# Optimization experiments

Hardware: AMD Instinct MI355X
Metric: run time of the kernel (lower is better)

## Reference

```python
import jax, jax.numpy as jnp
import numpy as np

N, E, IN, H, C, EDIM, G, NC = 20000, 200000, 512, 4, 64, 384, 64, 751
NEG_GATV2 = 0.2   # leaky_relu slope inside GATv2 attention
NEG_ACT = 0.01    # F.leaky_relu default between layers


def _w(key, shape):
    return jax.random.normal(key, shape, dtype=jnp.float32) * 0.05


def setup_inputs() -> dict:
    key = jax.random.key(0)
    ks = jax.random.split(key, 24)
    x = jax.random.normal(ks[0], (N, IN), dtype=jnp.float32)
    edge_index = jax.random.randint(ks[1], (2, E), 0, N, dtype=jnp.int32)
    edge_attr = jax.random.normal(ks[2], (E, EDIM), dtype=jnp.float32)
    batch = (jnp.arange(N, dtype=jnp.int32) * G) // N  # sorted, covers all G graphs
    return {
        "x": x, "edge_index": edge_index, "edge_attr": edge_attr, "batch": batch,
        # GATv2 layer 1 (512 -> 4 heads x 64, concat)
        "W1l": _w(ks[3], (IN, H * C)), "b1l": jnp.zeros((H * C,), jnp.float32),
        "W1r": _w(ks[4], (IN, H * C)), "b1r": jnp.zeros((H * C,), jnp.float32),
        "W1e": _w(ks[5], (EDIM, H * C)),
        "att1": _w(ks[6], (H, C)), "bias1": jnp.zeros((H * C,), jnp.float32),
        # GATv2 layer 2 (256 -> 1 head x 64)
        "W2l": _w(ks[7], (H * C, C)), "b2l": jnp.zeros((C,), jnp.float32),
        "W2r": _w(ks[8], (H * C, C)), "b2r": jnp.zeros((C,), jnp.float32),
        "W2e": _w(ks[9], (EDIM, C)),
        "att2": _w(ks[10], (1, C)), "bias2": jnp.zeros((C,), jnp.float32),
        # LayerNorm + classifier
        "ln_g": jnp.ones((C,), jnp.float32), "ln_b": jnp.zeros((C,), jnp.float32),
        "clf_W": _w(ks[11], (C, NC)), "clf_b": jnp.zeros((NC,), jnp.float32),
    }


def gatv2_layer(x, ei_i, ei_j, ea, Wl, bl, Wr, br, We, att, bias, heads, outc):
    n = x.shape[0]
    xl = (x @ Wl + bl).reshape(n, heads, outc)  # source-side transform (x_j)
    xr = (x @ Wr + br).reshape(n, heads, outc)  # target-side transform (x_i)
    ep = (ea @ We).reshape(-1, heads, outc)     # lin_edge has no bias in PyG
    m = jax.nn.leaky_relu(xl[ei_j] + xr[ei_i] + ep, NEG_GATV2)  # [E',H,C]
    logit = jnp.einsum('ehc,hc->eh', m, att)
    lmax = jax.ops.segment_max(logit, ei_i, num_segments=n)
    ex = jnp.exp(logit - lmax[ei_i])
    den = jax.ops.segment_sum(ex, ei_i, num_segments=n)
    alpha = ex / den[ei_i]                                       # segment softmax
    out = jax.ops.segment_sum(xl[ei_j] * alpha[:, :, None], ei_i, num_segments=n)
    return out.reshape(n, heads * outc) + bias, alpha


def reference(x, edge_index, edge_attr, batch, W1l, b1l, W1r, b1r, W1e, att1, bias1,
              W2l, b2l, W2r, b2r, W2e, att2, bias2, ln_g, ln_b, clf_W, clf_b):
    n = x.shape[0]
    row, col = edge_index[0], edge_index[1]
    # add_self_loops with fill_value='mean': loop attr = scatter-mean over edge_index[1]
    cnt = jax.ops.segment_sum(jnp.ones_like(edge_attr[:, 0]), col, num_segments=n)
    loop_attr = jax.ops.segment_sum(edge_attr, col, num_segments=n) / jnp.maximum(cnt, 1.0)[:, None]
    loops = jnp.arange(n, dtype=row.dtype)
    # flow='target_to_source': aggregate at i=edge_index[0], messages from j=edge_index[1]
    ei_i = jnp.concatenate([row, loops])
    ei_j = jnp.concatenate([col, loops])
    ea = jnp.concatenate([edge_attr, loop_attr], axis=0)

    h1, _ = gatv2_layer(x, ei_i, ei_j, ea, W1l, b1l, W1r, b1r, W1e, att1, bias1, H, C)
    h1 = jax.nn.leaky_relu(h1, NEG_ACT)
    h2, _ = gatv2_layer(h1, ei_i, ei_j, ea, W2l, b2l, W2r, b2r, W2e, att2, bias2, 1, C)
    h2 = jax.nn.leaky_relu(h2, NEG_ACT)

    g = jax.ops.segment_max(h2, batch, num_segments=G)  # global_max_pool -> [G, C]
    mu = g.mean(axis=-1, keepdims=True)
    var = g.var(axis=-1, keepdims=True)
    gn = (g - mu) / jnp.sqrt(var + 1e-5) * ln_g + ln_b
    cls_score = gn @ clf_W + clf_b
    return cls_score, gn
```

## Files before the change

### kernel.cpp

```cpp
#include <hip/hip_runtime.h>

#define NN 20000
#define NE 200000
#define NH1 256
#define ED 384
#define NG 64
#define NCLS 751
#define ETOT (NE + NN)

typedef unsigned short u16;
typedef __attribute__((ext_vector_type(8))) short short8;
typedef __attribute__((ext_vector_type(4))) float f32x4;

__device__ __forceinline__ float bf2f(u16 u){
  union { unsigned int i; float f; } v; v.i = ((unsigned int)u) << 16; return v.f;
}
__device__ __forceinline__ u16 f2bf(float f){
  union { float f; unsigned int i; } v; v.f = f;
  return (u16)((v.i + 0x7fffu + ((v.i >> 16) & 1u)) >> 16);
}

__global__ void transpose_k(const float* __restrict__ in, u16* __restrict__ out, int K, int N){
  int idx = blockIdx.x * 256 + threadIdx.x;
  if (idx >= K * N) return;
  int k = idx / N, n = idx - k * N;
  out[n * K + k] = f2bf(in[idx]);
}

__global__ void concatbias_k(const float* __restrict__ b1l, const float* __restrict__ b1r,
                             const float* __restrict__ b2l, const float* __restrict__ b2r,
                             float* __restrict__ biasLR1, float* __restrict__ biasLR2){
  int i = blockIdx.x * 256 + threadIdx.x;
  if (i < 256) biasLR1[i] = b1l[i];
  else if (i < 512) biasLR1[i] = b1r[i - 256];
  else if (i < 576) biasLR2[i - 512] = b2l[i - 512];
  else if (i < 640) biasLR2[i - 512] = b2r[i - 576];
}

__global__ void hist_k(const int* __restrict__ rowA, const int* __restrict__ colA,
                       int* __restrict__ degR, int* __restrict__ degC){
  int e = blockIdx.x * 256 + threadIdx.x;
  if (e >= NE) return;
  atomicAdd(&degR[rowA[e]], 1);
  atomicAdd(&degC[colA[e]], 1);
}

__global__ void scan_k(const int* __restrict__ degR, const int* __restrict__ degC,
                       int* __restrict__ rowPtr, int* __restrict__ colPtr){
  __shared__ int sR[256], sC[256];
  int t = threadIdx.x;
  const int chunk = (NN + 255) / 256;
  int beg = t * chunk, end = min(beg + chunk, NN);
  int aR = 0, aC = 0;
  for (int i = beg; i < end; i++){ aR += degR[i]; aC += degC[i]; }
  sR[t] = aR; sC[t] = aC;
  __syncthreads();
  for (int off = 1; off < 256; off <<= 1){
    int vR = 0, vC = 0;
    if (t >= off){ vR = sR[t - off]; vC = sC[t - off]; }
    __syncthreads();
    sR[t] += vR; sC[t] += vC;
    __syncthreads();
  }
  int rR = (t == 0) ? 0 : sR[t - 1];
  int rC = (t == 0) ? 0 : sC[t - 1];
  for (int i = beg; i < end; i++){
    rowPtr[i] = rR; rR += degR[i];
    colPtr[i] = rC; rC += degC[i];
  }
  if (t == 255){ rowPtr[NN] = sR[255]; colPtr[NN] = sC[255]; }
}

__global__ void scatter_k(const int* __restrict__ rowA, const int* __restrict__ colA,
                          const int* __restrict__ rowPtr, const int* __restrict__ colPtr,
                          int* __restrict__ rowCur, int* __restrict__ colCur,
                          int* __restrict__ rowIdx, int* __restrict__ colIdx){
  int e = blockIdx.x * 256 + threadIdx.x;
  if (e >= NE) return;
  int r = rowA[e]; int p = atomicAdd(&rowCur[r], 1); rowIdx[rowPtr[r] + p] = e;
  int c = colA[e]; int q = atomicAdd(&colCur[c], 1); colIdx[colPtr[c] + q] = e;
}

__global__ __launch_bounds__(256) void loopattr_k(const int* __restrict__ colPtr,
                                                  const int* __restrict__ colIdx,
                                                  const float* __restrict__ eattr,
                                                  u16* __restrict__ loopA16){
  int node = blockIdx.x * 4 + (threadIdx.x >> 6);
  if (node >= NN) return;
  int lane = threadIdx.x & 63;
  int p0 = colPtr[node], deg = colPtr[node + 1] - p0;
  float inv = 1.f / fmaxf((float)deg, 1.f);
  float s[6] = {0.f, 0.f, 0.f, 0.f, 0.f, 0.f};
  for (int t = 0; t < deg; t++){
    const float* rowp = eattr + (size_t)colIdx[p0 + t] * ED;
    #pragma unroll
    for (int c0 = 0; c0 < 6; c0++) s[c0] += rowp[c0 * 64 + lane];
  }
  u16* outp = loopA16 + (size_t)node * ED;
  #pragma unroll
  for (int c0 = 0; c0 < 6; c0++) outp[c0 * 64 + lane] = f2bf(s[c0] * inv);
}

__global__ __launch_bounds__(256)
void gemm_k(const void* __restrict__ Av, int aF32,
            const u16* __restrict__ Bt, int M, int K, int Ntot,
            const float* __restrict__ bias, u16* __restrict__ outBf)
{
  __shared__ __align__(16) u16 lA[128 * 40];
  __shared__ __align__(16) u16 lB[64 * 40];
  const int tid  = threadIdx.x;
  const int lane = tid & 63;
  const int wave = tid >> 6;
  const int m0 = blockIdx.x * 128;
  const int n0 = blockIdx.y * 64;
  const int lr  = tid >> 2;
  const int lkc = (tid & 3) << 3;
  const int lm = lane & 15;
  const int lk = (lane >> 4) << 3;
  const int wrow = wave << 5;

  f32x4 acc[2][4];
  #pragma unroll
  for (int i = 0; i < 2; i++)
    #pragma unroll
    for (int j = 0; j < 4; j++) acc[i][j] = (f32x4){0.f, 0.f, 0.f, 0.f};

  for (int k0 = 0; k0 < K; k0 += 32){
    #pragma unroll
    for (int p = 0; p < 2; p++){
      int row = lr + (p << 6);
      int gm = m0 + row;
      union { u16 h[8]; uint4 v; } pk;
      pk.v = make_uint4(0u, 0u, 0u, 0u);
      if (gm < M){
        if (aF32){
          const float* src = (const float*)Av + (size_t)gm * K + k0 + lkc;
          float4 f0 = *(const float4*)src;
          float4 f1 = *(const float4*)(src + 4);
          pk.h[0] = f2bf(f0.x); pk.h[1] = f2bf(f0.y); pk.h[2] = f2bf(f0.z); pk.h[3] = f2bf(f0.w);
          pk.h[4] = f2bf(f1.x); pk.h[5] = f2bf(f1.y); pk.h[6] = f2bf(f1.z); pk.h[7] = f2bf(f1.w);
        } else {
          pk.v = *(const uint4*)((const u16*)Av + (size_t)gm * K + k0 + lkc);
        }
      }
      *(uint4*)(&lA[row * 40 + lkc]) = pk.v;
    }
    *(uint4*)(&lB[lr * 40 + lkc]) = *(const uint4*)(Bt + (size_t)(n0 + lr) * K + k0 + lkc);
    __syncthreads();
    short8 a0 = *(const short8*)(&lA[(wrow + lm) * 40 + lk]);
    short8 a1 = *(const short8*)(&lA[(wrow + 16 + lm) * 40 + lk]);
    #pragma unroll
    for (int nj = 0; nj < 4; nj++){
      short8 b = *(const short8*)(&lB[(nj * 16 + lm) * 40 + lk]);
      acc[0][nj] = __builtin_amdgcn_mfma_f32_16x16x32_bf16(a0, b, acc[0][nj], 0, 0, 0);
      acc[1][nj] = __builtin_amdgcn_mfma_f32_16x16x32_bf16(a1, b, acc[1][nj], 0, 0, 0);
    }
    __syncthreads();
  }

  #pragma unroll
  for (int mi = 0; mi < 2; mi++)
    #pragma unroll
    for (int r4 = 0; r4 < 4; r4++){
      int row = wrow + mi * 16 + ((lane >> 4) << 2) + r4;
      int gm = m0 + row;
      if (gm < M){
        #pragma unroll
        for (int nj = 0; nj < 4; nj++){
          int gc = n0 + nj * 16 + lm;
          outBf[(size_t)gm * Ntot + gc] = f2bf(acc[mi][nj][r4] + bias[gc]);
        }
      }
    }
}

__global__ __launch_bounds__(256)
void edge_k(const float* __restrict__ eattr, const u16* __restrict__ loopA16,
            const u16* __restrict__ BtE,
            const int* __restrict__ rowA, const int* __restrict__ colA,
            const u16* __restrict__ XLR1,
            const float* __restrict__ att1,
            float* __restrict__ logit1,
            u16* __restrict__ ep2)
{
  __shared__ __align__(16) u16 lA[64 * 40];
  __shared__ __align__(16) u16 lB[320 * 40];
  const int tid = threadIdx.x;
  const int lane = tid & 63;
  const int wave = tid >> 6;
  const int m0 = blockIdx.x * 64;
  const int lm = lane & 15;
  const int lk = (lane >> 4) << 3;
  const int arow = tid >> 2;
  const int akc = (tid & 3) << 3;

  f32x4 acc[4][5];
  #pragma unroll
  for (int i = 0; i < 4; i++)
    #pragma unroll
    for (int j = 0; j < 5; j++) acc[i][j] = (f32x4){0.f, 0.f, 0.f, 0.f};

  const int gmA = m0 + arow;
  const int isF = (gmA < NE);
  const char* aBase = isF ? (const char*)(eattr + (size_t)gmA * ED)
                          : (const char*)(loopA16 + (size_t)(gmA - NE) * ED);
  const int aSh = isF ? 2 : 1;
  const u16* bBase = BtE + (size_t)arow * ED + akc;

  uint4 pA0, pA1, pB0, pB1, pB2, pB3, pB4;

#define EDGE_ISSUE(K0) \
  { size_t aoff = ((size_t)((K0) + akc)) << aSh; \
    pA0 = *(const uint4*)(aBase + aoff); \
    pA1 = *(const uint4*)(aBase + aoff + 16); \
    const u16* bp = bBase + (K0); \
    pB0 = *(const uint4*)(bp); \
    pB1 = *(const uint4*)(bp + (size_t)64 * ED); \
    pB2 = *(const uint4*)(bp + (size_t)128 * ED); \
    pB3 = *(const uint4*)(bp + (size_t)192 * ED); \
    pB4 = *(const uint4*)(bp + (size_t)256 * ED); }

#define EDGE_STORE \
  { union { u16 h[8]; uint4 v; } pk; \
    if (isF){ \
      const float* f0 = (const float*)&pA0; \
      const float* f1 = (const float*)&pA1; \
      pk.h[0] = f2bf(f0[0]); pk.h[1] = f2bf(f0[1]); pk.h[2] = f2bf(f0[2]); pk.h[3] = f2bf(f0[3]); \
      pk.h[4] = f2bf(f1[0]); pk.h[5] = f2bf(f1[1]); pk.h[6] = f2bf(f1[2]); pk.h[7] = f2bf(f1[3]); \
    } else { pk.v = pA0; } \
    *(uint4*)(&lA[arow * 40 + akc]) = pk.v; \
    *(uint4*)(&lB[(arow      ) * 40 + akc]) = pB0; \
    *(uint4*)(&lB[(arow +  64) * 40 + akc]) = pB1; \
    *(uint4*)(&lB[(arow + 128) * 40 + akc]) = pB2; \
    *(uint4*)(&lB[(arow + 192) * 40 + akc]) = pB3; \
    *(uint4*)(&lB[(arow + 256) * 40 + akc]) = pB4; }

  EDGE_ISSUE(0);
  for (int k0 = 0; k0 < ED; k0 += 32){
    EDGE_STORE;
    __syncthreads();
    if (k0 + 32 < ED) EDGE_ISSUE(k0 + 32);
    short8 a[4];
    #pragma unroll
    for (int mi = 0; mi < 4; mi++) a[mi] = *(const short8*)(&lA[(mi * 16 + lm) * 40 + lk]);
    #pragma unroll
    for (int nj = 0; nj < 4; nj++){
      short8 b = *(const short8*)(&lB[(wave * 64 + nj * 16 + lm) * 40 + lk]);
      #pragma unroll
      for (int mi = 0; mi < 4; mi++)
        acc[mi][nj] = __builtin_amdgcn_mfma_f32_16x16x32_bf16(a[mi], b, acc[mi][nj], 0, 0, 0);
    }
    {
      short8 b = *(const short8*)(&lB[(256 + wave * 16 + lm) * 40 + lk]);
      #pragma unroll
      for (int mi = 0; mi < 4; mi++)
        acc[mi][4] = __builtin_amdgcn_mfma_f32_16x16x32_bf16(a[mi], b, acc[mi][4], 0, 0, 0);
    }
    __syncthreads();
  }
#undef EDGE_ISSUE
#undef EDGE_STORE

  float attc[4];
  #pragma unroll
  for (int nj = 0; nj < 4; nj++) attc[nj] = att1[wave * 64 + nj * 16 + lm];
  const int quad4 = (lane >> 4) << 2;
  #pragma unroll
  for (int mi = 0; mi < 4; mi++)
    #pragma unroll
    for (int r4 = 0; r4 < 4; r4++){
      int e = m0 + mi * 16 + quad4 + r4;
      float partial = 0.f;
      if (e < ETOT){
        int ii = (e < NE) ? rowA[e] : (e - NE);
        int jj = (e < NE) ? colA[e] : (e - NE);
        const u16* xlp = XLR1 + (size_t)jj * 512 + wave * 64;
        const u16* xrp = XLR1 + (size_t)ii * 512 + 256 + wave * 64;
        #pragma unroll
        for (int nj = 0; nj < 4; nj++){
          float v = acc[mi][nj][r4] + bf2f(xlp[nj * 16 + lm]) + bf2f(xrp[nj * 16 + lm]);
          v = (v > 0.f) ? v : 0.2f * v;
          partial += v * attc[nj];
        }
        ep2[(size_t)e * 64 + wave * 16 + lm] = f2bf(acc[mi][4][r4]);
      }
      partial += __shfl_xor(partial, 1);
      partial += __shfl_xor(partial, 2);
      partial += __shfl_xor(partial, 4);
      partial += __shfl_xor(partial, 8);
      if (lm == 0 && e < ETOT) logit1[(size_t)e * 4 + wave] = partial;
    }
}

__global__ __launch_bounds__(256) void logit2_k(const int* __restrict__ rowA,
    const int* __restrict__ colA, const u16* __restrict__ ep2,
    const u16* __restrict__ XLR2,
    const float* __restrict__ att2, float* __restrict__ logit2)
{
  int e = blockIdx.x * 16 + (threadIdx.x >> 4);
  if (e >= ETOT) return;
  int lm = threadIdx.x & 15;
  int ii = (e < NE) ? rowA[e] : (e - NE);
  int jj = (e < NE) ? colA[e] : (e - NE);
  ushort4 pe = *(const ushort4*)(ep2 + (size_t)e * 64 + lm * 4);
  ushort4 pl = *(const ushort4*)(XLR2 + (size_t)jj * 128 + lm * 4);
  ushort4 pr = *(const ushort4*)(XLR2 + (size_t)ii * 128 + 64 + lm * 4);
  float s = 0.f;
  float v0 = bf2f(pe.x) + bf2f(pl.x) + bf2f(pr.x); v0 = v0 > 0.f ? v0 : 0.2f * v0;
  float v1 = bf2f(pe.y) + bf2f(pl.y) + bf2f(pr.y); v1 = v1 > 0.f ? v1 : 0.2f * v1;
  float v2 = bf2f(pe.z) + bf2f(pl.z) + bf2f(pr.z); v2 = v2 > 0.f ? v2 : 0.2f * v2;
  float v3 = bf2f(pe.w) + bf2f(pl.w) + bf2f(pr.w); v3 = v3 > 0.f ? v3 : 0.2f * v3;
  s = v0 * att2[lm * 4] + v1 * att2[lm * 4 + 1] + v2 * att2[lm * 4 + 2] + v3 * att2[lm * 4 + 3];
  s += __shfl_xor(s, 1);
  s += __shfl_xor(s, 2);
  s += __shfl_xor(s, 4);
  s += __shfl_xor(s, 8);
  if (lm == 0) logit2[e] = s;
}

__global__ __launch_bounds__(256) void agg1_k(const int* __restrict__ rowPtr,
    const int* __restrict__ rowIdx, const float4* __restrict__ lg4,
    const u16* __restrict__ XL1, int xstride, const int* __restrict__ colA,
    const float* __restrict__ bias1, u16* __restrict__ H1)
{
  int node = blockIdx.x * 4 + (threadIdx.x >> 6);
  if (node >= NN) return;
  int lane = threadIdx.x & 63;
  int p0 = rowPtr[node], deg = rowPtr[node + 1] - p0;
  float4 sl = lg4[NE + node];
  float m0 = sl.x, m1 = sl.y, m2 = sl.z, m3 = sl.w;
  for (int t = lane; t < deg; t += 64){
    float4 l = lg4[rowIdx[p0 + t]];
    m0 = fmaxf(m0, l.x); m1 = fmaxf(m1, l.y); m2 = fmaxf(m2, l.z); m3 = fmaxf(m3, l.w);
  }
  #pragma unroll
  for (int off = 32; off > 0; off >>= 1){
    m0 = fmaxf(m0, __shfl_xor(m0, off));
    m1 = fmaxf(m1, __shfl_xor(m1, off));
    m2 = fmaxf(m2, __shfl_xor(m2, off));
    m3 = fmaxf(m3, __shfl_xor(m3, off));
  }
  float d0, d1, d2, d3, a0, a1, a2, a3;
  {
    float e0 = __expf(sl.x - m0), e1 = __expf(sl.y - m1), e2 = __expf(sl.z - m2), e3 = __expf(sl.w - m3);
    d0 = e0; d1 = e1; d2 = e2; d3 = e3;
    const u16* xp = XL1 + (size_t)node * xstride;
    a0 = e0 * bf2f(xp[lane]); a1 = e1 * bf2f(xp[64 + lane]);
    a2 = e2 * bf2f(xp[128 + lane]); a3 = e3 * bf2f(xp[192 + lane]);
  }
  for (int t = 0; t < deg; t++){
    int e = rowIdx[p0 + t];
    float4 l = lg4[e];
    int j = colA[e];
    float e0 = __expf(l.x - m0), e1 = __expf(l.y - m1), e2 = __expf(l.z - m2), e3 = __expf(l.w - m3);
    d0 += e0; d1 += e1; d2 += e2; d3 += e3;
    const u16* xp = XL1 + (size_t)j * xstride;
    a0 += e0 * bf2f(xp[lane]); a1 += e1 * bf2f(xp[64 + lane]);
    a2 += e2 * bf2f(xp[128 + lane]); a3 += e3 * bf2f(xp[192 + lane]);
  }
  float v0 = a0 / d0 + bias1[lane];
  float v1 = a1 / d1 + bias1[64 + lane];
  float v2 = a2 / d2 + bias1[128 + lane];
  float v3 = a3 / d3 + bias1[192 + lane];
  v0 = v0 > 0.f ? v0 : 0.01f * v0;
  v1 = v1 > 0.f ? v1 : 0.01f * v1;
  v2 = v2 > 0.f ? v2 : 0.01f * v2;
  v3 = v3 > 0.f ? v3 : 0.01f * v3;
  u16* hp = H1 + (size_t)node * NH1;
  hp[lane] = f2bf(v0); hp[64 + lane] = f2bf(v1);
  hp[128 + lane] = f2bf(v2); hp[192 + lane] = f2bf(v3);
}

__global__ __launch_bounds__(256) void agg2_k(const int* __restrict__ rowPtr,
    const int* __restrict__ rowIdx, const float* __restrict__ lg,
    const u16* __restrict__ XL2, int xstride, const int* __restrict__ colA,
    const float* __restrict__ bias2, float* __restrict__ H2)
{
  int node = blockIdx.x * 4 + (threadIdx.x >> 6);
  if (node >= NN) return;
  int lane = threadIdx.x & 63;
  int p0 = rowPtr[node], deg = rowPtr[node + 1] - p0;
  float sl = lg[NE + node];
  float mx = sl;
  for (int t = lane; t < deg; t += 64) mx = fmaxf(mx, lg[rowIdx[p0 + t]]);
  #pragma unroll
  for (int off = 32; off > 0; off >>= 1) mx = fmaxf(mx, __shfl_xor(mx, off));
  float den = __expf(sl - mx);
  float acc = den * bf2f(XL2[(size_t)node * xstride + lane]);
  for (int t = 0; t < deg; t++){
    int e = rowIdx[p0 + t];
    float ex = __expf(lg[e] - mx);
    den += ex;
    acc += ex * bf2f(XL2[(size_t)colA[e] * xstride + lane]);
  }
  float v = acc / den + bias2[lane];
  v = v > 0.f ? v : 0.01f * v;
  H2[(size_t)node * 64 + lane] = v;
}

__global__ __launch_bounds__(256) void poolln_k(const float* __restrict__ H2,
    const float* __restrict__ lng, const float* __restrict__ lnb, float* __restrict__ outGn)
{
  __shared__ float sm[4][64];
  int g = blockIdx.x, w = threadIdx.x >> 6, c = threadIdx.x & 63;
  int beg = (g * NN + NG - 1) / NG;
  int end = ((g + 1) * NN + NG - 1) / NG;
  float m = -3.0e38f;
  for (int n = beg + w; n < end; n += 4) m = fmaxf(m, H2[(size_t)n * 64 + c]);
  sm[w][c] = m;
  __syncthreads();
  if (threadIdx.x < 64){
    m = fmaxf(fmaxf(sm[0][c], sm[1][c]), fmaxf(sm[2][c], sm[3][c]));
    float s = m;
    #pragma unroll
    for (int off = 32; off > 0; off >>= 1) s += __shfl_xor(s, off);
    float mu = s * (1.f / 64.f);
    float d = m - mu;
    float vv = d * d;
    #pragma unroll
    for (int off = 32; off > 0; off >>= 1) vv += __shfl_xor(vv, off);
    float var = vv * (1.f / 64.f);
    outGn[g * 64 + c] = d * rsqrtf(var + 1e-5f) * lng[c] + lnb[c];
  }
}

__global__ __launch_bounds__(256) void clf_k(const float* __restrict__ gn,
    const float* __restrict__ W, const float* __restrict__ b, float* __restrict__ outCls)
{
  __shared__ float sg[64];
  int g = blockIdx.x;
  if (threadIdx.x < 64) sg[threadIdx.x] = gn[g * 64 + threadIdx.x];
  __syncthreads();
  for (int o = threadIdx.x; o < NCLS; o += 256){
    float s = b[o];
    #pragma unroll 16
    for (int c = 0; c < 64; c++) s += sg[c] * W[c * NCLS + o];
    outCls[(size_t)g * NCLS + o] = s;
  }
}

extern "C" void kernel_launch(void* const* d_in, const int* in_sizes, int n_in,
                              void* d_out, int out_size, void* d_ws, size_t ws_size,
                              hipStream_t stream)
{
  const float* x     = (const float*)d_in[0];
  const int*   eidx  = (const int*)d_in[1];
  const float* eattr = (const float*)d_in[2];
  const float* W1l = (const float*)d_in[4];
  const float* b1l = (const float*)d_in[5];
  const float* W1r = (const float*)d_in[6];
  const float* b1r = (const float*)d_in[7];
  const float* W1e = (const float*)d_in[8];
  const float* att1 = (const float*)d_in[9];
  const float* bias1 = (const float*)d_in[10];
  const float* W2l = (const float*)d_in[11];
  const float* b2l = (const float*)d_in[12];
  const float* W2r = (const float*)d_in[13];
  const float* b2r = (const float*)d_in[14];
  const float* W2e = (const float*)d_in[15];
  const float* att2 = (const float*)d_in[16];
  const float* bias2 = (const float*)d_in[17];
  const float* lng = (const float*)d_in[18];
  const float* lnb = (const float*)d_in[19];
  const float* clfW = (const float*)d_in[20];
  const float* clfb = (const float*)d_in[21];
  const int* rowA = eidx;
  const int* colA = eidx + NE;

  char* w = (char*)d_ws;
  auto alloc = [&](size_t b) -> char* {
    char* p = w; w += (b + 255) & ~(size_t)255; return p;
  };
  u16* W1lrT  = (u16*)alloc((size_t)512 * 512 * 2);
  u16* BtE    = (u16*)alloc((size_t)320 * ED * 2);
  u16* W2lrT  = (u16*)alloc((size_t)128 * 256 * 2);
  float* biasLR1 = (float*)alloc(512 * 4);
  float* biasLR2 = (float*)alloc(128 * 4);
  int* degR   = (int*)alloc((size_t)NN * 4);
  int* degC   = (int*)alloc((size_t)NN * 4);
  int* rowPtr = (int*)alloc((size_t)(NN + 1) * 4);
  int* colPtr = (int*)alloc((size_t)(NN + 1) * 4);
  int* rowCur = (int*)alloc((size_t)NN * 4);
  int* colCur = (int*)alloc((size_t)NN * 4);
  int* rowIdx = (int*)alloc((size_t)NE * 4);
  int* colIdx = (int*)alloc((size_t)NE * 4);
  char* loopRegion = alloc((size_t)NN * ED * 2);
  u16* loopA16 = (u16*)loopRegion;
  u16* XLR1   = (u16*)alloc((size_t)NN * 512 * 2);
  float* logit1 = (float*)alloc((size_t)ETOT * 4 * 4);
  u16* H1     = (u16*)alloc((size_t)NN * NH1 * 2);
  u16* ep2    = (u16*)alloc((size_t)ETOT * 64 * 2);
  u16* XLR2   = (u16*)loopRegion;
  float* logit2 = (float*)(loopRegion + (size_t)5500928);
  float* H2   = (float*)(loopRegion + (size_t)6553600);

  hipMemsetAsync(degR, 0, (size_t)NN * 4, stream);
  hipMemsetAsync(degC, 0, (size_t)NN * 4, stream);
  hipMemsetAsync(rowCur, 0, (size_t)NN * 4, stream);
  hipMemsetAsync(colCur, 0, (size_t)NN * 4, stream);

  transpose_k<<<(512 * 256 + 255) / 256, 256, 0, stream>>>(W1l, W1lrT, 512, 256);
  transpose_k<<<(512 * 256 + 255) / 256, 256, 0, stream>>>(W1r, W1lrT + (size_t)256 * 512, 512, 256);
  transpose_k<<<(ED * 256 + 255) / 256, 256, 0, stream>>>(W1e, BtE, ED, 256);
  transpose_k<<<(ED * 64 + 255) / 256, 256, 0, stream>>>(W2e, BtE + (size_t)256 * ED, ED, 64);
  transpose_k<<<(256 * 64 + 255) / 256, 256, 0, stream>>>(W2l, W2lrT, 256, 64);
  transpose_k<<<(256 * 64 + 255) / 256, 256, 0, stream>>>(W2r, W2lrT + (size_t)64 * 256, 256, 64);
  concatbias_k<<<3, 256, 0, stream>>>(b1l, b1r, b2l, b2r, biasLR1, biasLR2);

  hist_k<<<(NE + 255) / 256, 256, 0, stream>>>(rowA, colA, degR, degC);
  scan_k<<<1, 256, 0, stream>>>(degR, degC, rowPtr, colPtr);
  scatter_k<<<(NE + 255) / 256, 256, 0, stream>>>(rowA, colA, rowPtr, colPtr,
                                                  rowCur, colCur, rowIdx, colIdx);
  loopattr_k<<<(NN + 3) / 4, 256, 0, stream>>>(colPtr, colIdx, eattr, loopA16);

  dim3 gx1((NN + 127) / 128, 8);
  gemm_k<<<gx1, 256, 0, stream>>>(x, 1, W1lrT, NN, 512, 512, biasLR1, XLR1);
  edge_k<<<(ETOT + 63) / 64, 256, 0, stream>>>(eattr, loopA16, BtE, rowA, colA,
                                               XLR1, att1, logit1, ep2);
  agg1_k<<<(NN + 3) / 4, 256, 0, stream>>>(rowPtr, rowIdx, (const float4*)logit1,
                                           XLR1, 512, colA, bias1, H1);
  dim3 gx2((NN + 127) / 128, 2);
  gemm_k<<<gx2, 256, 0, stream>>>(H1, 0, W2lrT, NN, 256, 128, biasLR2, XLR2);
  logit2_k<<<(ETOT + 15) / 16, 256, 0, stream>>>(rowA, colA, ep2, XLR2, att2, logit2);
  agg2_k<<<(NN + 3) / 4, 256, 0, stream>>>(rowPtr, rowIdx, logit2, XLR2, 128, colA, bias2, H2);

  float* outCls = (float*)d_out;
  float* outGn  = outCls + (size_t)NG * NCLS;
  poolln_k<<<NG, 256, 0, stream>>>(H2, lng, lnb, outGn);
  clf_k<<<NG, 256, 0, stream>>>(outGn, clfW, clfb, outCls);
}
```

Baseline: 967.1 us.

## Pre-convert inputs to bf16, prefetch GEMM tiles, unroll aggregation loops

Adds a pass that converts x to bf16 once, and makes the loop-attribute kernel also write every edge attribute as bf16 into one contiguous buffer alongside the self-loop rows. The node GEMM and the edge GEMM then read half-width A operands with no branching or conversion in their inner loops. The GEMM also gains register prefetch of the next K tile, and both aggregation kernels process two neighbours per iteration to expose more memory-level parallelism. This trades extra conversion passes and a larger workspace for less repeated fp32 traffic. The GEMM's row bounds guard on loads is removed, so the last tile reads past the end of the valid rows into adjacent workspace.

```diff
diff --git a/kernel.cpp b/kernel.cpp
--- a/kernel.cpp
+++ b/kernel.cpp
@@ -25,6 +25,17 @@
   if (idx >= K * N) return;
   int k = idx / N, n = idx - k * N;
   out[n * K + k] = f2bf(in[idx]);
+}
+
+__global__ void convx_k(const float* __restrict__ in, u16* __restrict__ out, int total8){
+  int idx = blockIdx.x * 256 + threadIdx.x;
+  if (idx >= total8) return;
+  const float4* p = (const float4*)in + (size_t)idx * 2;
+  float4 f0 = p[0], f1 = p[1];
+  union { u16 h[8]; uint4 v; } pk;
+  pk.h[0] = f2bf(f0.x); pk.h[1] = f2bf(f0.y); pk.h[2] = f2bf(f0.z); pk.h[3] = f2bf(f0.w);
+  pk.h[4] = f2bf(f1.x); pk.h[5] = f2bf(f1.y); pk.h[6] = f2bf(f1.z); pk.h[7] = f2bf(f1.w);
+  ((uint4*)out)[idx] = pk.v;
 }
 
 __global__ void concatbias_k(const float* __restrict__ b1l, const float* __restrict__ b1r,
@@ -84,7 +95,7 @@
 __global__ __launch_bounds__(256) void loopattr_k(const int* __restrict__ colPtr,
                                                   const int* __restrict__ colIdx,
                                                   const float* __restrict__ eattr,
-                                                  u16* __restrict__ loopA16){
+                                                  u16* __restrict__ ea16){
   int node = blockIdx.x * 4 + (threadIdx.x >> 6);
   if (node >= NN) return;
   int lane = threadIdx.x & 63;
@@ -92,17 +103,23 @@
   float inv = 1.f / fmaxf((float)deg, 1.f);
   float s[6] = {0.f, 0.f, 0.f, 0.f, 0.f, 0.f};
   for (int t = 0; t < deg; t++){
-    const float* rowp = eattr + (size_t)colIdx[p0 + t] * ED;
-    #pragma unroll
-    for (int c0 = 0; c0 < 6; c0++) s[c0] += rowp[c0 * 64 + lane];
-  }
-  u16* outp = loopA16 + (size_t)node * ED;
+    int e = colIdx[p0 + t];
+    const float* rowp = eattr + (size_t)e * ED;
+    u16* wp = ea16 + (size_t)e * ED;
+    #pragma unroll
+    for (int c0 = 0; c0 < 6; c0++){
+      float v = rowp[c0 * 64 + lane];
+      s[c0] += v;
+      wp[c0 * 64 + lane] = f2bf(v);
+    }
+  }
+  u16* outp = ea16 + (size_t)(NE + node) * ED;
   #pragma unroll
   for (int c0 = 0; c0 < 6; c0++) outp[c0 * 64 + lane] = f2bf(s[c0] * inv);
 }
 
 __global__ __launch_bounds__(256)
-void gemm_k(const void* __restrict__ Av, int aF32,
+void gemm_k(const u16* __restrict__ A16,
             const u16* __restrict__ Bt, int M, int K, int Ntot,
             const float* __restrict__ bias, u16* __restrict__ outBf)
 {
@@ -125,28 +142,24 @@
     #pragma unroll
     for (int j = 0; j < 4; j++) acc[i][j] = (f32x4){0.f, 0.f, 0.f, 0.f};
 
+  const u16* aB0 = A16 + (size_t)(m0 + lr) * K + lkc;
+  const u16* aB1 = A16 + (size_t)(m0 + lr + 64) * K + lkc;
+  const u16* bB  = Bt + (size_t)(n0 + lr) * K + lkc;
+
+  uint4 rA0, rA1, rB;
+
+#define GEMM_ISSUE(K0) \
+  { rA0 = *(const uint4*)(aB0 + (K0)); \
+    rA1 = *(const uint4*)(aB1 + (K0)); \
+    rB  = *(const uint4*)(bB  + (K0)); }
+
+  GEMM_ISSUE(0);
   for (int k0 = 0; k0 < K; k0 += 32){
-    #pragma unroll
-    for (int p = 0; p < 2; p++){
-      int row = lr + (p << 6);
-      int gm = m0 + row;
-      union { u16 h[8]; uint4 v; } pk;
-      pk.v = make_uint4(0u, 0u, 0u, 0u);
-      if (gm < M){
-        if (aF32){
-          const float* src = (const float*)Av + (size_t)gm * K + k0 + lkc;
-          float4 f0 = *(const float4*)src;
-          float4 f1 = *(const float4*)(src + 4);
-          pk.h[0] = f2bf(f0.x); pk.h[1] = f2bf(f0.y); pk.h[2] = f2bf(f0.z); pk.h[3] = f2bf(f0.w);
-          pk.h[4] = f2bf(f1.x); pk.h[5] = f2bf(f1.y); pk.h[6] = f2bf(f1.z); pk.h[7] = f2bf(f1.w);
-        } else {
-          pk.v = *(const uint4*)((const u16*)Av + (size_t)gm * K + k0 + lkc);
-        }
-      }
-      *(uint4*)(&lA[row * 40 + lkc]) = pk.v;
-    }
-    *(uint4*)(&lB[lr * 40 + lkc]) = *(const uint4*)(Bt + (size_t)(n0 + lr) * K + k0 + lkc);
+    *(uint4*)(&lA[lr * 40 + lkc]) = rA0;
+    *(uint4*)(&lA[(lr + 64) * 40 + lkc]) = rA1;
+    *(uint4*)(&lB[lr * 40 + lkc]) = rB;
     __syncthreads();
+    if (k0 + 32 < K) GEMM_ISSUE(k0 + 32);
     short8 a0 = *(const short8*)(&lA[(wrow + lm) * 40 + lk]);
     short8 a1 = *(const short8*)(&lA[(wrow + 16 + lm) * 40 + lk]);
     #pragma unroll
@@ -157,6 +170,7 @@
     }
     __syncthreads();
   }
+#undef GEMM_ISSUE
 
   #pragma unroll
   for (int mi = 0; mi < 2; mi++)
@@ -175,7 +189,7 @@
 }
 
 __global__ __launch_bounds__(256)
-void edge_k(const float* __restrict__ eattr, const u16* __restrict__ loopA16,
+void edge_k(const u16* __restrict__ ea16,
             const u16* __restrict__ BtE,
             const int* __restrict__ rowA, const int* __restrict__ colA,
             const u16* __restrict__ XLR1,
@@ -201,18 +215,13 @@
     for (int j = 0; j < 5; j++) acc[i][j] = (f32x4){0.f, 0.f, 0.f, 0.f};
 
   const int gmA = m0 + arow;
-  const int isF = (gmA < NE);
-  const char* aBase = isF ? (const char*)(eattr + (size_t)gmA * ED)
-                          : (const char*)(loopA16 + (size_t)(gmA - NE) * ED);
-  const int aSh = isF ? 2 : 1;
+  const u16* aBase = ea16 + (size_t)gmA * ED + akc;
   const u16* bBase = BtE + (size_t)arow * ED + akc;
 
-  uint4 pA0, pA1, pB0, pB1, pB2, pB3, pB4;
+  uint4 pA, pB0, pB1, pB2, pB3, pB4;
 
 #define EDGE_ISSUE(K0) \
-  { size_t aoff = ((size_t)((K0) + akc)) << aSh; \
-    pA0 = *(const uint4*)(aBase + aoff); \
-    pA1 = *(const uint4*)(aBase + aoff + 16); \
+  { pA  = *(const uint4*)(aBase + (K0)); \
     const u16* bp = bBase + (K0); \
     pB0 = *(const uint4*)(bp); \
     pB1 = *(const uint4*)(bp + (size_t)64 * ED); \
@@ -220,24 +229,14 @@
     pB3 = *(const uint4*)(bp + (size_t)192 * ED); \
     pB4 = *(const uint4*)(bp + (size_t)256 * ED); }
 
-#define EDGE_STORE \
-  { union { u16 h[8]; uint4 v; } pk; \
-    if (isF){ \
-      const float* f0 = (const float*)&pA0; \
-      const float* f1 = (const float*)&pA1; \
-      pk.h[0] = f2bf(f0[0]); pk.h[1] = f2bf(f0[1]); pk.h[2] = f2bf(f0[2]); pk.h[3] = f2bf(f0[3]); \
-      pk.h[4] = f2bf(f1[0]); pk.h[5] = f2bf(f1[1]); pk.h[6] = f2bf(f1[2]); pk.h[7] = f2bf(f1[3]); \
-    } else { pk.v = pA0; } \
-    *(uint4*)(&lA[arow * 40 + akc]) = pk.v; \
-    *(uint4*)(&lB[(arow      ) * 40 + akc]) = pB0; \
-    *(uint4*)(&lB[(arow +  64) * 40 + akc]) = pB1; \
-    *(uint4*)(&lB[(arow + 128) * 40 + akc]) = pB2; \
-    *(uint4*)(&lB[(arow + 192) * 40 + akc]) = pB3; \
-    *(uint4*)(&lB[(arow + 256) * 40 + akc]) = pB4; }
-
   EDGE_ISSUE(0);
   for (int k0 = 0; k0 < ED; k0 += 32){
-    EDGE_STORE;
+    *(uint4*)(&lA[arow * 40 + akc]) = pA;
+    *(uint4*)(&lB[(arow      ) * 40 + akc]) = pB0;
+    *(uint4*)(&lB[(arow +  64) * 40 + akc]) = pB1;
+    *(uint4*)(&lB[(arow + 128) * 40 + akc]) = pB2;
+    *(uint4*)(&lB[(arow + 192) * 40 + akc]) = pB3;
+    *(uint4*)(&lB[(arow + 256) * 40 + akc]) = pB4;
     __syncthreads();
     if (k0 + 32 < ED) EDGE_ISSUE(k0 + 32);
     short8 a[4];
@@ -259,7 +258,6 @@
     __syncthreads();
   }
 #undef EDGE_ISSUE
-#undef EDGE_STORE
 
   float attc[4];
   #pragma unroll
@@ -348,7 +346,25 @@
     a0 = e0 * bf2f(xp[lane]); a1 = e1 * bf2f(xp[64 + lane]);
     a2 = e2 * bf2f(xp[128 + lane]); a3 = e3 * bf2f(xp[192 + lane]);
   }
-  for (int t = 0; t < deg; t++){
+  int t = 0;
+  for (; t + 1 < deg; t += 2){
+    int eA = rowIdx[p0 + t];
+    int eB = rowIdx[p0 + t + 1];
+    float4 lA_ = lg4[eA];
+    float4 lB_ = lg4[eB];
+    int jA = colA[eA];
+    int jB = colA[eB];
+    const u16* xa = XL1 + (size_t)jA * xstride;
+    const u16* xb = XL1 + (size_t)jB * xstride;
+    float eA0 = __expf(lA_.x - m0), eA1 = __expf(lA_.y - m1), eA2 = __expf(lA_.z - m2), eA3 = __expf(lA_.w - m3);
+    float eB0 = __expf(lB_.x - m0), eB1 = __expf(lB_.y - m1), eB2 = __expf(lB_.z - m2), eB3 = __expf(lB_.w - m3);
+    d0 += eA0 + eB0; d1 += eA1 + eB1; d2 += eA2 + eB2; d3 += eA3 + eB3;
+    a0 += eA0 * bf2f(xa[lane])       + eB0 * bf2f(xb[lane]);
+    a1 += eA1 * bf2f(xa[64 + lane])  + eB1 * bf2f(xb[64 + lane]);
+    a2 += eA2 * bf2f(xa[128 + lane]) + eB2 * bf2f(xb[128 + lane]);
+    a3 += eA3 * bf2f(xa[192 + lane]) + eB3 * bf2f(xb[192 + lane]);
+  }
+  if (t < deg){
     int e = rowIdx[p0 + t];
     float4 l = lg4[e];
     int j = colA[e];
@@ -387,7 +403,19 @@
   for (int off = 32; off > 0; off >>= 1) mx = fmaxf(mx, __shfl_xor(mx, off));
   float den = __expf(sl - mx);
   float acc = den * bf2f(XL2[(size_t)node * xstride + lane]);
-  for (int t = 0; t < deg; t++){
+  int t = 0;
+  for (; t + 1 < deg; t += 2){
+    int eA = rowIdx[p0 + t];
+    int eB = rowIdx[p0 + t + 1];
+    float exA = __expf(lg[eA] - mx);
+    float exB = __expf(lg[eB] - mx);
+    int jA = colA[eA];
+    int jB = colA[eB];
+    den += exA + exB;
+    acc += exA * bf2f(XL2[(size_t)jA * xstride + lane])
+         + exB * bf2f(XL2[(size_t)jB * xstride + lane]);
+  }
+  if (t < deg){
     int e = rowIdx[p0 + t];
     float ex = __expf(lg[e] - mx);
     den += ex;
@@ -484,15 +512,15 @@
   int* colCur = (int*)alloc((size_t)NN * 4);
   int* rowIdx = (int*)alloc((size_t)NE * 4);
   int* colIdx = (int*)alloc((size_t)NE * 4);
-  char* loopRegion = alloc((size_t)NN * ED * 2);
-  u16* loopA16 = (u16*)loopRegion;
+  u16* ea16   = (u16*)alloc((size_t)ETOT * ED * 2);
+  u16* x16    = (u16*)alloc((size_t)NN * 512 * 2);
   u16* XLR1   = (u16*)alloc((size_t)NN * 512 * 2);
   float* logit1 = (float*)alloc((size_t)ETOT * 4 * 4);
   u16* H1     = (u16*)alloc((size_t)NN * NH1 * 2);
   u16* ep2    = (u16*)alloc((size_t)ETOT * 64 * 2);
-  u16* XLR2   = (u16*)loopRegion;
-  float* logit2 = (float*)(loopRegion + (size_t)5500928);
-  float* H2   = (float*)(loopRegion + (size_t)6553600);
+  u16* XLR2   = (u16*)ea16;
+  float* logit2 = (float*)((char*)ea16 + (size_t)5500928);
+  float* H2   = (float*)((char*)ea16 + (size_t)6553600);
 
   hipMemsetAsync(degR, 0, (size_t)NN * 4, stream);
   hipMemsetAsync(degC, 0, (size_t)NN * 4, stream);
@@ -506,21 +534,22 @@
   transpose_k<<<(256 * 64 + 255) / 256, 256, 0, stream>>>(W2l, W2lrT, 256, 64);
   transpose_k<<<(256 * 64 + 255) / 256, 256, 0, stream>>>(W2r, W2lrT + (size_t)64 * 256, 256, 64);
   concatbias_k<<<3, 256, 0, stream>>>(b1l, b1r, b2l, b2r, biasLR1, biasLR2);
+  convx_k<<<(NN * 512 / 8 + 255) / 256, 256, 0, stream>>>(x, x16, NN * 512 / 8);
 
   hist_k<<<(NE + 255) / 256, 256, 0, stream>>>(rowA, colA, degR, degC);
   scan_k<<<1, 256, 0, stream>>>(degR, degC, rowPtr, colPtr);
   scatter_k<<<(NE + 255) / 256, 256, 0, stream>>>(rowA, colA, rowPtr, colPtr,
                                                   rowCur, colCur, rowIdx, colIdx);
-  loopattr_k<<<(NN + 3) / 4, 256, 0, stream>>>(colPtr, colIdx, eattr, loopA16);
+  loopattr_k<<<(NN + 3) / 4, 256, 0, stream>>>(colPtr, colIdx, eattr, ea16);
 
   dim3 gx1((NN + 127) / 128, 8);
-  gemm_k<<<gx1, 256, 0, stream>>>(x, 1, W1lrT, NN, 512, 512, biasLR1, XLR1);
-  edge_k<<<(ETOT + 63) / 64, 256, 0, stream>>>(eattr, loopA16, BtE, rowA, colA,
+  gemm_k<<<gx1, 256, 0, stream>>>(x16, W1lrT, NN, 512, 512, biasLR1, XLR1);
+  edge_k<<<(ETOT + 63) / 64, 256, 0, stream>>>(ea16, BtE, rowA, colA,
                                                XLR1, att1, logit1, ep2);
   agg1_k<<<(NN + 3) / 4, 256, 0, stream>>>(rowPtr, rowIdx, (const float4*)logit1,
                                            XLR1, 512, colA, bias1, H1);
   dim3 gx2((NN + 127) / 128, 2);
-  gemm_k<<<gx2, 256, 0, stream>>>(H1, 0, W2lrT, NN, 256, 128, biasLR2, XLR2);
+  gemm_k<<<gx2, 256, 0, stream>>>(H1, W2lrT, NN, 256, 128, biasLR2, XLR2);
   logit2_k<<<(ETOT + 15) / 16, 256, 0, stream>>>(rowA, colA, ep2, XLR2, att2, logit2);
   agg2_k<<<(NN + 3) / 4, 256, 0, stream>>>(rowPtr, rowIdx, logit2, XLR2, 128, colA, bias2, H2);
 
```

New measurement: 962.7 us. About the same (-0.5%).
